# Performance work log

Measured on AMD Instinct MI355X. Metric: run time of the kernel, lower is better.

The kernel has to match this reference:

```python
import jax, jax.numpy as jnp
import numpy as np
from jax import lax

# dims
B, N, D, H, K, NS = 16, 4096, 64, 128, 32, 1024  # clouds, pts/cloud, feat, hidden, max neighbors, fps samples
R = 0.2  # radius


def _fps(pos, n_s):
    """Farthest point sampling on one cloud. pos: [N,3] -> idx [n_s] int32."""
    n = pos.shape[0]

    def step(carry, _):
        dist, last = carry
        d = jnp.sum((pos - pos[last]) ** 2, axis=-1)
        dist = jnp.minimum(dist, d)
        nxt = jnp.argmax(dist).astype(jnp.int32)
        return (dist, nxt), last

    init = (jnp.full((n,), 1e10, pos.dtype), jnp.int32(0))
    _, idx = lax.scan(step, init, None, length=n_s)
    return idx


def setup_inputs() -> dict:
    key = jax.random.key(0)
    ks = jax.random.split(key, 6)
    s1 = 1.0 / np.sqrt(D + 1)
    s2 = 1.0 / np.sqrt(H)
    s3 = 1.0 / np.sqrt(D + H)
    return {
        "x": jax.random.normal(ks[0], (B, N, D), jnp.float32),
        "pos": jax.random.uniform(ks[1], (B, N, 3), jnp.float32),
        "W1": jax.random.normal(ks[2], (D + 1, H), jnp.float32) * s1,
        "b1": jnp.zeros((H,), jnp.float32),
        "W2": jax.random.normal(ks[3], (H, 3), jnp.float32) * s2,
        "b2": jnp.zeros((3,), jnp.float32),
        "W3": jax.random.normal(ks[4], (D + H, H), jnp.float32) * s3,
        "b3": jnp.zeros((H,), jnp.float32),
    }


def reference(x, pos, W1, b1, W2, b2, W3, b3):
    # 1) FPS downsample per cloud -> centers
    idx = jax.vmap(lambda p: _fps(p, NS))(pos)                    # [B,NS]
    pos_s = jax.vmap(lambda p, i: p[i])(pos, idx)                 # [B,NS,3]

    # 2) radius neighbor search: nearest-K within R (<= max_num_neighbors=32)
    d2 = jnp.sum((pos_s[:, :, None, :] - pos[:, None, :, :]) ** 2, axis=-1)  # [B,NS,N]
    masked = jnp.where(d2 <= R * R, d2, jnp.inf)
    neg, nbr = lax.top_k(-masked, K)                              # nearest K
    valid = (-neg) <= R * R                                       # [B,NS,K]

    # 3) gather neighbor features/positions
    x_j = jax.vmap(lambda a, i: a[i])(x, nbr)                     # [B,NS,K,D]
    pos_j = jax.vmap(lambda a, i: a[i])(pos, nbr)                 # [B,NS,K,3]
    diff = pos_j - pos_s[:, :, None, :]                           # pos_j - pos_i
    d2sel = jnp.sum(diff ** 2, axis=-1)
    dist = jnp.where(d2sel > 0, jnp.sqrt(jnp.where(d2sel > 0, d2sel, 1.0)), 0.0)

    # 4) message MLPs
    feat = jnp.concatenate([x_j, dist[..., None]], axis=-1)       # [B,NS,K,D+1]
    emb = jax.nn.relu(feat @ W1 + b1)                             # nn_msg_x
    pw = emb @ W2 + b2                                            # nn_msg_pos
    pmsg = diff * pw

    # 5) masked aggregate: sum for x, mean for pos
    m = valid[..., None].astype(emb.dtype)
    aggr_x = jnp.sum(emb * m, axis=2)                             # [B,NS,H]
    cnt = jnp.maximum(jnp.sum(m, axis=2), 1.0)                    # [B,NS,1]
    aggr_pos = jnp.sum(pmsg * m, axis=2) / cnt                    # [B,NS,3]

    # 6) update
    x_d = jax.vmap(lambda a, i: a[i])(x, idx)                     # [B,NS,D]
    out_x = jax.nn.relu(jnp.concatenate([x_d, aggr_x], axis=-1) @ W3 + b3)
    out_pos = pos_s + aggr_pos
    return out_x, out_pos, idx
```

## Files before the change

### kernel.cpp

```cpp
#include <hip/hip_runtime.h>
#include <math.h>

#define B_ 16
#define N_ 4096
#define D_ 64
#define H_ 128
#define K_ 32
#define NS_ 1024
#define R2_ 0.04f
#define CAP_ 1024

typedef short short8 __attribute__((ext_vector_type(8)));
typedef float f32x4 __attribute__((ext_vector_type(4)));
typedef unsigned short ushort_t;

static __device__ __forceinline__ short f2bf(float f) {
    unsigned u = __float_as_uint(f);
    unsigned r = (u + 0x7FFFu + ((u >> 16) & 1u)) >> 16;
    return (short)r;
}

template<int CTRL, int RM>
static __device__ __forceinline__ unsigned dppmov(unsigned v) {
    return (unsigned)__builtin_amdgcn_update_dpp((int)v, (int)v, CTRL, RM, 0xF, false);
}

#define DPP_FMAX_STEP(CTRL, RM)                                           \
    {                                                                     \
        float n = __uint_as_float(dppmov<CTRL, RM>(__float_as_uint(wm))); \
        wm = fmaxf(wm, n);                                                \
    }

#define DPP_UMIN_STEP(CTRL, RM)                                           \
    {                                                                     \
        unsigned n = dppmov<CTRL, RM>(cand);                              \
        cand = n < cand ? n : cand;                                       \
    }

#define DPP_UMIN_STEP_V(var, CTRL, RM)                                    \
    {                                                                     \
        unsigned n = dppmov<CTRL, RM>(var);                               \
        var = n < var ? n : var;                                          \
    }

__global__ __launch_bounds__(256) void cvt_kernel(
    const float* __restrict__ x, ushort_t* __restrict__ xb)
{
    const size_t i = ((size_t)blockIdx.x * 256 + threadIdx.x) * 8;
    float4 a = *(const float4*)(x + i);
    float4 c = *(const float4*)(x + i + 4);
    short8 o;
    o[0] = f2bf(a.x); o[1] = f2bf(a.y); o[2] = f2bf(a.z); o[3] = f2bf(a.w);
    o[4] = f2bf(c.x); o[5] = f2bf(c.y); o[6] = f2bf(c.z); o[7] = f2bf(c.w);
    *(short8*)(xb + i) = o;
}

__global__ __launch_bounds__(256, 1) void fps_kernel(
    const float* __restrict__ pos, int* __restrict__ idx_i,
    float* __restrict__ idx_f, float* __restrict__ pos_s)
{
    __shared__ float4 lpos4[N_];
    __shared__ float4 sres[NS_];
    __shared__ unsigned long long skey[2][4];
    __shared__ float4 scoord[2][4];
    const int b = blockIdx.x;
    const int t = threadIdx.x;
    const int wv = t >> 6;
    const int lane = t & 63;
    const float* posb = pos + (size_t)b * N_ * 3;
    for (int p = t; p < N_; p += 256)
        lpos4[p] = make_float4(posb[3 * p + 0], posb[3 * p + 1], posb[3 * p + 2], 0.f);
    __syncthreads();

    float px[16], py[16], pz[16], dist[16];
#pragma unroll
    for (int j = 0; j < 16; ++j) {
        float4 v = lpos4[t + 256 * j];
        px[j] = v.x; py[j] = v.y; pz[j] = v.z;
        dist[j] = 1e10f;
    }
    unsigned curidx = 0;
    float4 c0 = lpos4[0];
    float ccx = c0.x, ccy = c0.y, ccz = c0.z;

    for (int ns = 0; ns < NS_; ++ns) {
        if (t == 0)
            sres[ns] = make_float4(ccx, ccy, ccz, __uint_as_float(curidx));
        float bv = -1.f; int bj = 0;
#pragma unroll
        for (int j = 0; j < 16; ++j) {
            float dx = __fsub_rn(px[j], ccx);
            float dy = __fsub_rn(py[j], ccy);
            float dz = __fsub_rn(pz[j], ccz);
            float d2 = __fadd_rn(__fadd_rn(__fmul_rn(dx, dx), __fmul_rn(dy, dy)), __fmul_rn(dz, dz));
            float dn = fminf(dist[j], d2);
            dist[j] = dn;
            bool g = dn > bv;
            bv = g ? dn : bv;
            bj = g ? j : bj;
        }
        float wm = bv;
        DPP_FMAX_STEP(0x111, 0xF)
        DPP_FMAX_STEP(0x112, 0xF)
        DPP_FMAX_STEP(0x114, 0xF)
        DPP_FMAX_STEP(0x118, 0xF)
        DPP_FMAX_STEP(0x142, 0xA)
        DPP_FMAX_STEP(0x143, 0xC)
        const float wavemax = __uint_as_float(
            (unsigned)__builtin_amdgcn_readlane((int)__float_as_uint(wm), 63));
        const unsigned pidx = (unsigned)t + ((unsigned)bj << 8);
        const unsigned long long mask = __ballot(bv == wavemax);
        unsigned widx;
        if (__popcll(mask) == 1) {
            const int wl = __ffsll((long long)mask) - 1;
            widx = (unsigned)__builtin_amdgcn_readlane((int)pidx, wl);
        } else {
            unsigned cand = (bv == wavemax) ? pidx : 0xFFFFFFFFu;
            DPP_UMIN_STEP(0x111, 0xF)
            DPP_UMIN_STEP(0x112, 0xF)
            DPP_UMIN_STEP(0x114, 0xF)
            DPP_UMIN_STEP(0x118, 0xF)
            DPP_UMIN_STEP(0x142, 0xA)
            DPP_UMIN_STEP(0x143, 0xC)
            widx = (unsigned)__builtin_amdgcn_readlane((int)cand, 63);
        }
        float4 wc = lpos4[widx];
        if (lane == 0) {
            skey[ns & 1][wv] = (((unsigned long long)__float_as_uint(wavemax)) << 32)
                             | (unsigned long long)(0xFFFFFFFFu - widx);
            scoord[ns & 1][wv] = wc;
        }
        __syncthreads();
        {
            unsigned sid = (unsigned)(lane & 3);
            unsigned long long skv = skey[ns & 1][sid];
            float4 scv = scoord[ns & 1][sid];
            unsigned kh2 = (unsigned)(skv >> 32), kl2 = (unsigned)skv;
#define SLOT_STEP(CTRL)                                                        \
            {                                                                  \
                unsigned nh = dppmov<CTRL, 0xF>(kh2);                          \
                unsigned nl = dppmov<CTRL, 0xF>(kl2);                          \
                unsigned nsid = dppmov<CTRL, 0xF>(sid);                        \
                unsigned long long nk = (((unsigned long long)nh) << 32) | nl; \
                unsigned long long ok = (((unsigned long long)kh2) << 32) | kl2;\
                if (nk > ok) { kh2 = nh; kl2 = nl; sid = nsid; }               \
            }
            SLOT_STEP(0x101)
            SLOT_STEP(0x102)
#undef SLOT_STEP
            const int slotwin = __builtin_amdgcn_readfirstlane((int)sid);
            curidx = 0xFFFFFFFFu - (unsigned)__builtin_amdgcn_readfirstlane((int)kl2);
            ccx = __uint_as_float((unsigned)__builtin_amdgcn_readlane(
                      (int)__float_as_uint(scv.x), slotwin));
            ccy = __uint_as_float((unsigned)__builtin_amdgcn_readlane(
                      (int)__float_as_uint(scv.y), slotwin));
            ccz = __uint_as_float((unsigned)__builtin_amdgcn_readlane(
                      (int)__float_as_uint(scv.z), slotwin));
        }
    }
    __syncthreads();
    for (int i = t; i < NS_; i += 256) {
        float4 r = sres[i];
        unsigned id = __float_as_uint(r.w);
        idx_i[b * NS_ + i] = (int)id;
        idx_f[b * NS_ + i] = (float)id;
        pos_s[(b * NS_ + i) * 3 + 0] = r.x;
        pos_s[(b * NS_ + i) * 3 + 1] = r.y;
        pos_s[(b * NS_ + i) * 3 + 2] = r.z;
    }
}

__global__ __launch_bounds__(256) void nbr_kernel(
    const float* __restrict__ pos, const float* __restrict__ pos_s,
    int* __restrict__ nbr, float* __restrict__ cntv)
{
    __shared__ unsigned long long ck[4][CAP_];
    const int w = threadIdx.x >> 6;
    const int lane = threadIdx.x & 63;
    const int s = blockIdx.x * 4 + w;
    const int b = s >> 10;
    const float cx = pos_s[s * 3 + 0], cy = pos_s[s * 3 + 1], cz = pos_s[s * 3 + 2];
    const float* posb = pos + (size_t)b * N_ * 3;
    int m = 0;
    for (int base = 0; base < N_; base += 64) {
        int p = base + lane;
        float dx = __fsub_rn(posb[3 * p + 0], cx);
        float dy = __fsub_rn(posb[3 * p + 1], cy);
        float dz = __fsub_rn(posb[3 * p + 2], cz);
        float d2 = __fadd_rn(__fadd_rn(__fmul_rn(dx, dx), __fmul_rn(dy, dy)), __fmul_rn(dz, dz));
        bool in = (d2 <= R2_);
        unsigned long long msk = __ballot(in);
        int before = __popcll(msk & ((1ull << lane) - 1ull));
        int slot = m + before;
        if (in && slot < CAP_)
            ck[w][slot] = ((unsigned long long)__float_as_uint(d2) << 32) | (unsigned)p;
        m += __popcll(msk);
    }
    if (m > CAP_) m = CAP_;
    __asm__ volatile("s_waitcnt lgkmcnt(0)" ::: "memory");
    int kcnt = m < K_ ? m : K_;
    if (m <= 256) {
        unsigned long long kr[4];
#pragma unroll
        for (int r = 0; r < 4; ++r) {
            int q = r * 64 + lane;
            unsigned long long v = ck[w][q & (CAP_ - 1)];
            kr[r] = (q < m) ? v : ~0ull;
        }
        unsigned chosen = 0;
        for (int k = 0; k < kcnt; ++k) {
            unsigned long long localk = ~0ull; int br = -1;
#pragma unroll
            for (int r = 0; r < 4; ++r) {
                bool ok = (!((chosen >> r) & 1u)) && (kr[r] < localk);
                localk = ok ? kr[r] : localk;
                br = ok ? r : br;
            }
            const unsigned mybits = (unsigned)(localk >> 32);
            const unsigned myidx = (unsigned)localk;
            unsigned wb = mybits;
            DPP_UMIN_STEP_V(wb, 0x111, 0xF)
            DPP_UMIN_STEP_V(wb, 0x112, 0xF)
            DPP_UMIN_STEP_V(wb, 0x114, 0xF)
            DPP_UMIN_STEP_V(wb, 0x118, 0xF)
            DPP_UMIN_STEP_V(wb, 0x142, 0xA)
            DPP_UMIN_STEP_V(wb, 0x143, 0xC)
            const unsigned minbits = (unsigned)__builtin_amdgcn_readlane((int)wb, 63);
            const unsigned long long wmask = __ballot(mybits == minbits);
            unsigned widx;
            if (__popcll(wmask) == 1) {
                const int wl = __ffsll((long long)wmask) - 1;
                widx = (unsigned)__builtin_amdgcn_readlane((int)myidx, wl);
            } else {
                unsigned cand = (mybits == minbits) ? myidx : 0xFFFFFFFFu;
                DPP_UMIN_STEP(0x111, 0xF)
                DPP_UMIN_STEP(0x112, 0xF)
                DPP_UMIN_STEP(0x114, 0xF)
                DPP_UMIN_STEP(0x118, 0xF)
                DPP_UMIN_STEP(0x142, 0xA)
                DPP_UMIN_STEP(0x143, 0xC)
                widx = (unsigned)__builtin_amdgcn_readlane((int)cand, 63);
            }
            if (mybits == minbits && myidx == widx) chosen |= 1u << br;
            if (lane == 0) nbr[s * K_ + k] = (int)widx;
        }
    } else {
        unsigned chosen = 0;
        for (int k = 0; k < kcnt; ++k) {
            unsigned long long localk = ~0ull; int bslot = -1;
            for (int r = 0; r * 64 + lane < m; ++r) {
                if (chosen & (1u << r)) continue;
                int q = r * 64 + lane;
                unsigned long long key = ck[w][q];
                if (key < localk) { localk = key; bslot = q; }
            }
            unsigned kh = (unsigned)(localk >> 32), kl = (unsigned)localk;
#define DPP_MIN_STEP2(CTRL, RM)                                           \
            {                                                             \
                unsigned nh = dppmov<CTRL, RM>(kh);                       \
                unsigned nl = dppmov<CTRL, RM>(kl);                       \
                unsigned long long nk = (((unsigned long long)nh) << 32) | nl; \
                unsigned long long ok = (((unsigned long long)kh) << 32) | kl; \
                if (nk < ok) { kh = nh; kl = nl; }                        \
            }
            DPP_MIN_STEP2(0x111, 0xF)
            DPP_MIN_STEP2(0x112, 0xF)
            DPP_MIN_STEP2(0x114, 0xF)
            DPP_MIN_STEP2(0x118, 0xF)
            DPP_MIN_STEP2(0x142, 0xA)
            DPP_MIN_STEP2(0x143, 0xC)
#undef DPP_MIN_STEP2
            unsigned mh = (unsigned)__builtin_amdgcn_readlane((int)kh, 63);
            unsigned ml = (unsigned)__builtin_amdgcn_readlane((int)kl, 63);
            unsigned long long bk = (((unsigned long long)mh) << 32) | ml;
            if (localk == bk && bslot >= 0) chosen |= 1u << (bslot >> 6);
            if (lane == 0) nbr[s * K_ + k] = (int)(bk & 0xFFFFFFFFull);
        }
    }
    if (lane == 0) {
        for (int k = kcnt; k < K_; ++k) nbr[s * K_ + k] = -1;
        cntv[s] = (float)kcnt;
    }
}

__global__ __launch_bounds__(256) void msg_kernel(
    const ushort_t* __restrict__ xb, const float* __restrict__ pos,
    const float* __restrict__ W1, const float* __restrict__ b1,
    const float* __restrict__ W2, const float* __restrict__ b2,
    const float* __restrict__ pos_s, const int* __restrict__ nbr,
    const float* __restrict__ cntv, float* __restrict__ aggr_x,
    float* __restrict__ out_pos)
{
    __shared__ __align__(16) char smem[4 * 5120];
    const int t = threadIdx.x;
    const int wv = t >> 6, lane = t & 63;
    const int quad = lane >> 4, cl = lane & 15;
    char* wb = smem + wv * 5120;

    short8 bfrag[8][2];
    float b1v[8], w1dv[8], w2v0[8], w2v1[8], w2v2[8];
#pragma unroll
    for (int Nt = 0; Nt < 8; ++Nt) {
        const int h = Nt * 16 + cl;
#pragma unroll
        for (int ks = 0; ks < 2; ++ks) {
            short8 f;
#pragma unroll
            for (int jj = 0; jj < 8; ++jj)
                f[jj] = f2bf(W1[(ks * 32 + quad * 8 + jj) * H_ + h]);
            bfrag[Nt][ks] = f;
        }
        b1v[Nt] = b1[h];
        w1dv[Nt] = W1[64 * H_ + h];
        w2v0[Nt] = W2[h * 3 + 0];
        w2v1[Nt] = W2[h * 3 + 1];
        w2v2[Nt] = W2[h * 3 + 2];
    }
    const float b20 = b2[0], b21 = b2[1], b22 = b2[2];

    const int kkg = lane >> 1, half = lane & 1;
    for (int i = 0; i < 4; ++i) {
        const int s = blockIdx.x * 16 + wv * 4 + i;
        const int b = s >> 10;
        const int n = nbr[s * K_ + kkg];
        {
            char* frow = wb + kkg * 144 + half * 64;
            if (n >= 0) {
                const short8* xr = (const short8*)(xb + ((size_t)b * N_ + n) * D_) + half * 4;
#pragma unroll
                for (int q = 0; q < 4; ++q) *(short8*)(frow + q * 16) = xr[q];
            } else {
                short8 z = {0, 0, 0, 0, 0, 0, 0, 0};
#pragma unroll
                for (int q = 0; q < 4; ++q) *(short8*)(frow + q * 16) = z;
            }
            if (half == 0) {
                float dxm = 0.f, dym = 0.f, dzm = 0.f, de = -1.f;
                if (n >= 0) {
                    const float* pj = pos + ((size_t)b * N_ + n) * 3;
                    float dx = pj[0] - pos_s[s * 3 + 0];
                    float dy = pj[1] - pos_s[s * 3 + 1];
                    float dz = pj[2] - pos_s[s * 3 + 2];
                    float d2 = dx * dx + dy * dy + dz * dz;
                    de = d2 > 0.f ? sqrtf(d2) : 0.f;
                    dxm = dx; dym = dy; dzm = dz;
                }
                f32x4 sv = {dxm, dym, dzm, de};
                *(f32x4*)(wb + 4608 + kkg * 16) = sv;
            }
        }
        float agp[8] = {0, 0, 0, 0, 0, 0, 0, 0};
        float gp0[8] = {0, 0, 0, 0, 0, 0, 0, 0};
        float gp1[8] = {0, 0, 0, 0, 0, 0, 0, 0};
        float gp2[8] = {0, 0, 0, 0, 0, 0, 0, 0};
#pragma unroll
        for (int Mt = 0; Mt < 2; ++Mt) {
            short8 a0 = *(short8*)(wb + (Mt * 16 + cl) * 144 + quad * 16);
            short8 a1 = *(short8*)(wb + (Mt * 16 + cl) * 144 + 64 + quad * 16);
            f32x4 acc[8];
#pragma unroll
            for (int Nt = 0; Nt < 8; ++Nt) {
                f32x4 z = {0.f, 0.f, 0.f, 0.f};
                z = __builtin_amdgcn_mfma_f32_16x16x32_bf16(a0, bfrag[Nt][0], z, 0, 0, 0);
                z = __builtin_amdgcn_mfma_f32_16x16x32_bf16(a1, bfrag[Nt][1], z, 0, 0, 0);
                acc[Nt] = z;
            }
            f32x4 sd[4];
#pragma unroll
            for (int r = 0; r < 4; ++r)
                sd[r] = *(f32x4*)(wb + 4608 + (Mt * 16 + quad * 4 + r) * 16);
#pragma unroll
            for (int Nt = 0; Nt < 8; ++Nt) {
#pragma unroll
                for (int r = 0; r < 4; ++r) {
                    float dr = sd[r][3];
                    float wgt = dr >= 0.f ? 1.f : 0.f;
                    float dd = dr >= 0.f ? dr : 0.f;
                    float e = fmaf(dd, w1dv[Nt], acc[Nt][r]) + b1v[Nt];
                    e = e > 0.f ? e : 0.f;
                    agp[Nt] = fmaf(wgt, e, agp[Nt]);
                    gp0[Nt] = fmaf(sd[r][0], e, gp0[Nt]);
                    gp1[Nt] = fmaf(sd[r][1], e, gp1[Nt]);
                    gp2[Nt] = fmaf(sd[r][2], e, gp2[Nt]);
                }
            }
        }
#pragma unroll
        for (int Nt = 0; Nt < 8; ++Nt) {
            float v = agp[Nt]; v += __shfl_xor(v, 16); v += __shfl_xor(v, 32);
            aggr_x[(size_t)s * H_ + Nt * 16 + cl] = v;
            float g0 = gp0[Nt]; g0 += __shfl_xor(g0, 16); g0 += __shfl_xor(g0, 32); gp0[Nt] = g0;
            float g1 = gp1[Nt]; g1 += __shfl_xor(g1, 16); g1 += __shfl_xor(g1, 32); gp1[Nt] = g1;
            float g2 = gp2[Nt]; g2 += __shfl_xor(g2, 16); g2 += __shfl_xor(g2, 32); gp2[Nt] = g2;
        }
        float pr0 = 0.f, pr1 = 0.f, pr2 = 0.f;
#pragma unroll
        for (int Nt = 0; Nt < 8; ++Nt) {
            pr0 = fmaf(w2v0[Nt], gp0[Nt], pr0);
            pr1 = fmaf(w2v1[Nt], gp1[Nt], pr1);
            pr2 = fmaf(w2v2[Nt], gp2[Nt], pr2);
        }
#pragma unroll
        for (int off = 1; off < 16; off <<= 1) {
            pr0 += __shfl_xor(pr0, off);
            pr1 += __shfl_xor(pr1, off);
            pr2 += __shfl_xor(pr2, off);
        }
        f32x4 dsv = *(f32x4*)(wb + 4608 + (lane & 31) * 16);
        float q0 = dsv[0], q1 = dsv[1], q2 = dsv[2];
#pragma unroll
        for (int off = 1; off < 32; off <<= 1) {
            q0 += __shfl_xor(q0, off);
            q1 += __shfl_xor(q1, off);
            q2 += __shfl_xor(q2, off);
        }
        float cnt = cntv[s]; if (cnt < 1.f) cnt = 1.f;
        if (lane < 3) {
            float pr = lane == 0 ? pr0 : (lane == 1 ? pr1 : pr2);
            float qq = lane == 0 ? q0 : (lane == 1 ? q1 : q2);
            float bb = lane == 0 ? b20 : (lane == 1 ? b21 : b22);
            out_pos[s * 3 + lane] = pos_s[s * 3 + lane] + (pr + bb * qq) / cnt;
        }
    }
}

__global__ __launch_bounds__(128) void out_kernel(
    const float* __restrict__ x, const float* __restrict__ W3,
    const float* __restrict__ b3, const int* __restrict__ idx_i,
    const float* __restrict__ aggr_x, float* __restrict__ out_x)
{
    __shared__ float rows[32][208];
    const int t = threadIdx.x;
    const int s0 = blockIdx.x * 32;
    const int sl = t >> 2, part = t & 3;
    const int s = s0 + sl;
    const int b = s >> 10;
    const int id = idx_i[s];
    {
        const float4* xr = (const float4*)(x + ((size_t)b * N_ + id) * D_);
        float4* rr = (float4*)&rows[sl][0];
#pragma unroll
        for (int q = 0; q < 4; ++q) rr[part * 4 + q] = xr[part * 4 + q];
        const float4* ar = (const float4*)(aggr_x + (size_t)s * H_);
        float4* rr2 = (float4*)&rows[sl][64];
#pragma unroll
        for (int q = 0; q < 8; ++q) rr2[part * 8 + q] = ar[part * 8 + q];
    }
    __syncthreads();
    float acc[32];
#pragma unroll
    for (int i = 0; i < 32; ++i) acc[i] = 0.f;
    for (int j4 = 0; j4 < 48; ++j4) {
        float w0 = W3[(j4 * 4 + 0) * H_ + t];
        float w1 = W3[(j4 * 4 + 1) * H_ + t];
        float w2 = W3[(j4 * 4 + 2) * H_ + t];
        float w3 = W3[(j4 * 4 + 3) * H_ + t];
#pragma unroll
        for (int i = 0; i < 32; ++i) {
            const float4 f = *(const float4*)&rows[i][j4 * 4];
            float a = acc[i];
            a = fmaf(f.x, w0, a); a = fmaf(f.y, w1, a);
            a = fmaf(f.z, w2, a); a = fmaf(f.w, w3, a);
            acc[i] = a;
        }
    }
    const float bb = b3[t];
#pragma unroll
    for (int i = 0; i < 32; ++i) {
        float v = acc[i] + bb;
        v = v > 0.f ? v : 0.f;
        out_x[(size_t)(s0 + i) * H_ + t] = v;
    }
}

extern "C" void kernel_launch(void* const* d_in, const int* in_sizes, int n_in,
                              void* d_out, int out_size, void* d_ws, size_t ws_size,
                              hipStream_t stream) {
    const float* x   = (const float*)d_in[0];
    const float* pos = (const float*)d_in[1];
    const float* W1  = (const float*)d_in[2];
    const float* b1  = (const float*)d_in[3];
    const float* W2  = (const float*)d_in[4];
    const float* b2  = (const float*)d_in[5];
    const float* W3  = (const float*)d_in[6];
    const float* b3  = (const float*)d_in[7];

    float* out_x   = (float*)d_out;
    float* out_pos = (float*)d_out + 2097152;
    float* idx_f   = (float*)d_out + 2146304;

    char* ws = (char*)d_ws;
    int*      idx_i  = (int*)ws;
    float*    pos_s  = (float*)(ws + 65536);
    int*      nbr    = (int*)(ws + 262144);
    float*    cntv   = (float*)(ws + 2359296);
    float*    aggr_x = (float*)(ws + 2424832);
    ushort_t* x_bf16 = (ushort_t*)(ws + 10813440);

    cvt_kernel<<<(B_ * N_ * D_) / (256 * 8), 256, 0, stream>>>(x, x_bf16);
    fps_kernel<<<B_, 256, 0, stream>>>(pos, idx_i, idx_f, pos_s);
    nbr_kernel<<<(B_ * NS_) / 4, 256, 0, stream>>>(pos, pos_s, nbr, cntv);
    msg_kernel<<<(B_ * NS_) / 16, 256, 0, stream>>>(x_bf16, pos, W1, b1, W2, b2,
                                                    pos_s, nbr, cntv, aggr_x, out_pos);
    out_kernel<<<(B_ * NS_) / 32, 128, 0, stream>>>(x, W3, b3, idx_i, aggr_x, out_x);
}
```

Baseline: 968.3 us.

## Fuse all stages into a persistent mega-kernel with FPS progress flags

Replaces the five kernel launches with one kernel. A ticket counter assigns the first 16 blocks to FPS, and these publish progress every 64 samples through release atomics. The other 1024 blocks each handle 16 centers and wait on that progress, then run the neighbor search, message MLP and output MLP inside the block. The aim is to overlap the serial FPS with downstream work and to drop the intermediate global buffers (nbr, cntv, aggr_x, bf16 copy of x). In exchange it relies on forward progress of spinning blocks, converts x to bf16 again at every neighbor gather, and runs the output GEMM at lower per-block parallelism.

```diff
diff --git a/kernel.cpp b/kernel.cpp
--- a/kernel.cpp
+++ b/kernel.cpp
@@ -12,7 +12,6 @@
 
 typedef short short8 __attribute__((ext_vector_type(8)));
 typedef float f32x4 __attribute__((ext_vector_type(4)));
-typedef unsigned short ushort_t;
 
 static __device__ __forceinline__ short f2bf(float f) {
     unsigned u = __float_as_uint(f);
@@ -43,196 +42,82 @@
         var = n < var ? n : var;                                          \
     }
 
-__global__ __launch_bounds__(256) void cvt_kernel(
-    const float* __restrict__ x, ushort_t* __restrict__ xb)
+__global__ __launch_bounds__(256, 1) void mega_kernel(
+    const float* __restrict__ pos, const float* __restrict__ x,
+    const float* __restrict__ W1, const float* __restrict__ b1,
+    const float* __restrict__ W2, const float* __restrict__ b2,
+    const float* __restrict__ W3, const float* __restrict__ b3,
+    int* ticket, int* progress, int* idx_i, float* pos_s,
+    float* out_x, float* out_pos, float* idx_f)
 {
-    const size_t i = ((size_t)blockIdx.x * 256 + threadIdx.x) * 8;
-    float4 a = *(const float4*)(x + i);
-    float4 c = *(const float4*)(x + i + 4);
-    short8 o;
-    o[0] = f2bf(a.x); o[1] = f2bf(a.y); o[2] = f2bf(a.z); o[3] = f2bf(a.w);
-    o[4] = f2bf(c.x); o[5] = f2bf(c.y); o[6] = f2bf(c.z); o[7] = f2bf(c.w);
-    *(short8*)(xb + i) = o;
-}
-
-__global__ __launch_bounds__(256, 1) void fps_kernel(
-    const float* __restrict__ pos, int* __restrict__ idx_i,
-    float* __restrict__ idx_f, float* __restrict__ pos_s)
-{
-    __shared__ float4 lpos4[N_];
-    __shared__ float4 sres[NS_];
-    __shared__ unsigned long long skey[2][4];
-    __shared__ float4 scoord[2][4];
-    const int b = blockIdx.x;
+    __shared__ __align__(16) char smem[66048];
+    __shared__ int srole;
     const int t = threadIdx.x;
+    if (t == 0) srole = atomicAdd(ticket, 1);
+    __syncthreads();
+    const int my = srole;
     const int wv = t >> 6;
     const int lane = t & 63;
-    const float* posb = pos + (size_t)b * N_ * 3;
-    for (int p = t; p < N_; p += 256)
-        lpos4[p] = make_float4(posb[3 * p + 0], posb[3 * p + 1], posb[3 * p + 2], 0.f);
-    __syncthreads();
-
-    float px[16], py[16], pz[16], dist[16];
-#pragma unroll
-    for (int j = 0; j < 16; ++j) {
-        float4 v = lpos4[t + 256 * j];
-        px[j] = v.x; py[j] = v.y; pz[j] = v.z;
-        dist[j] = 1e10f;
-    }
-    unsigned curidx = 0;
-    float4 c0 = lpos4[0];
-    float ccx = c0.x, ccy = c0.y, ccz = c0.z;
-
-    for (int ns = 0; ns < NS_; ++ns) {
-        if (t == 0)
-            sres[ns] = make_float4(ccx, ccy, ccz, __uint_as_float(curidx));
-        float bv = -1.f; int bj = 0;
+
+    if (my < B_) {
+        float4* lpos4 = (float4*)smem;
+        unsigned long long (*skey)[4] = (unsigned long long (*)[4])(smem + 65536);
+        float4 (*scoord)[4] = (float4 (*)[4])(smem + 65536 + 64);
+        const int b = my;
+        const float* posb = pos + (size_t)b * N_ * 3;
+        for (int p = t; p < N_; p += 256)
+            lpos4[p] = make_float4(posb[3 * p + 0], posb[3 * p + 1], posb[3 * p + 2], 0.f);
+        __syncthreads();
+
+        float px[16], py[16], pz[16], dist[16];
 #pragma unroll
         for (int j = 0; j < 16; ++j) {
-            float dx = __fsub_rn(px[j], ccx);
-            float dy = __fsub_rn(py[j], ccy);
-            float dz = __fsub_rn(pz[j], ccz);
-            float d2 = __fadd_rn(__fadd_rn(__fmul_rn(dx, dx), __fmul_rn(dy, dy)), __fmul_rn(dz, dz));
-            float dn = fminf(dist[j], d2);
-            dist[j] = dn;
-            bool g = dn > bv;
-            bv = g ? dn : bv;
-            bj = g ? j : bj;
-        }
-        float wm = bv;
-        DPP_FMAX_STEP(0x111, 0xF)
-        DPP_FMAX_STEP(0x112, 0xF)
-        DPP_FMAX_STEP(0x114, 0xF)
-        DPP_FMAX_STEP(0x118, 0xF)
-        DPP_FMAX_STEP(0x142, 0xA)
-        DPP_FMAX_STEP(0x143, 0xC)
-        const float wavemax = __uint_as_float(
-            (unsigned)__builtin_amdgcn_readlane((int)__float_as_uint(wm), 63));
-        const unsigned pidx = (unsigned)t + ((unsigned)bj << 8);
-        const unsigned long long mask = __ballot(bv == wavemax);
-        unsigned widx;
-        if (__popcll(mask) == 1) {
-            const int wl = __ffsll((long long)mask) - 1;
-            widx = (unsigned)__builtin_amdgcn_readlane((int)pidx, wl);
-        } else {
-            unsigned cand = (bv == wavemax) ? pidx : 0xFFFFFFFFu;
-            DPP_UMIN_STEP(0x111, 0xF)
-            DPP_UMIN_STEP(0x112, 0xF)
-            DPP_UMIN_STEP(0x114, 0xF)
-            DPP_UMIN_STEP(0x118, 0xF)
-            DPP_UMIN_STEP(0x142, 0xA)
-            DPP_UMIN_STEP(0x143, 0xC)
-            widx = (unsigned)__builtin_amdgcn_readlane((int)cand, 63);
-        }
-        float4 wc = lpos4[widx];
-        if (lane == 0) {
-            skey[ns & 1][wv] = (((unsigned long long)__float_as_uint(wavemax)) << 32)
-                             | (unsigned long long)(0xFFFFFFFFu - widx);
-            scoord[ns & 1][wv] = wc;
-        }
-        __syncthreads();
-        {
-            unsigned sid = (unsigned)(lane & 3);
-            unsigned long long skv = skey[ns & 1][sid];
-            float4 scv = scoord[ns & 1][sid];
-            unsigned kh2 = (unsigned)(skv >> 32), kl2 = (unsigned)skv;
-#define SLOT_STEP(CTRL)                                                        \
-            {                                                                  \
-                unsigned nh = dppmov<CTRL, 0xF>(kh2);                          \
-                unsigned nl = dppmov<CTRL, 0xF>(kl2);                          \
-                unsigned nsid = dppmov<CTRL, 0xF>(sid);                        \
-                unsigned long long nk = (((unsigned long long)nh) << 32) | nl; \
-                unsigned long long ok = (((unsigned long long)kh2) << 32) | kl2;\
-                if (nk > ok) { kh2 = nh; kl2 = nl; sid = nsid; }               \
-            }
-            SLOT_STEP(0x101)
-            SLOT_STEP(0x102)
-#undef SLOT_STEP
-            const int slotwin = __builtin_amdgcn_readfirstlane((int)sid);
-            curidx = 0xFFFFFFFFu - (unsigned)__builtin_amdgcn_readfirstlane((int)kl2);
-            ccx = __uint_as_float((unsigned)__builtin_amdgcn_readlane(
-                      (int)__float_as_uint(scv.x), slotwin));
-            ccy = __uint_as_float((unsigned)__builtin_amdgcn_readlane(
-                      (int)__float_as_uint(scv.y), slotwin));
-            ccz = __uint_as_float((unsigned)__builtin_amdgcn_readlane(
-                      (int)__float_as_uint(scv.z), slotwin));
-        }
-    }
-    __syncthreads();
-    for (int i = t; i < NS_; i += 256) {
-        float4 r = sres[i];
-        unsigned id = __float_as_uint(r.w);
-        idx_i[b * NS_ + i] = (int)id;
-        idx_f[b * NS_ + i] = (float)id;
-        pos_s[(b * NS_ + i) * 3 + 0] = r.x;
-        pos_s[(b * NS_ + i) * 3 + 1] = r.y;
-        pos_s[(b * NS_ + i) * 3 + 2] = r.z;
-    }
-}
-
-__global__ __launch_bounds__(256) void nbr_kernel(
-    const float* __restrict__ pos, const float* __restrict__ pos_s,
-    int* __restrict__ nbr, float* __restrict__ cntv)
-{
-    __shared__ unsigned long long ck[4][CAP_];
-    const int w = threadIdx.x >> 6;
-    const int lane = threadIdx.x & 63;
-    const int s = blockIdx.x * 4 + w;
-    const int b = s >> 10;
-    const float cx = pos_s[s * 3 + 0], cy = pos_s[s * 3 + 1], cz = pos_s[s * 3 + 2];
-    const float* posb = pos + (size_t)b * N_ * 3;
-    int m = 0;
-    for (int base = 0; base < N_; base += 64) {
-        int p = base + lane;
-        float dx = __fsub_rn(posb[3 * p + 0], cx);
-        float dy = __fsub_rn(posb[3 * p + 1], cy);
-        float dz = __fsub_rn(posb[3 * p + 2], cz);
-        float d2 = __fadd_rn(__fadd_rn(__fmul_rn(dx, dx), __fmul_rn(dy, dy)), __fmul_rn(dz, dz));
-        bool in = (d2 <= R2_);
-        unsigned long long msk = __ballot(in);
-        int before = __popcll(msk & ((1ull << lane) - 1ull));
-        int slot = m + before;
-        if (in && slot < CAP_)
-            ck[w][slot] = ((unsigned long long)__float_as_uint(d2) << 32) | (unsigned)p;
-        m += __popcll(msk);
-    }
-    if (m > CAP_) m = CAP_;
-    __asm__ volatile("s_waitcnt lgkmcnt(0)" ::: "memory");
-    int kcnt = m < K_ ? m : K_;
-    if (m <= 256) {
-        unsigned long long kr[4];
-#pragma unroll
-        for (int r = 0; r < 4; ++r) {
-            int q = r * 64 + lane;
-            unsigned long long v = ck[w][q & (CAP_ - 1)];
-            kr[r] = (q < m) ? v : ~0ull;
-        }
-        unsigned chosen = 0;
-        for (int k = 0; k < kcnt; ++k) {
-            unsigned long long localk = ~0ull; int br = -1;
-#pragma unroll
-            for (int r = 0; r < 4; ++r) {
-                bool ok = (!((chosen >> r) & 1u)) && (kr[r] < localk);
-                localk = ok ? kr[r] : localk;
-                br = ok ? r : br;
-            }
-            const unsigned mybits = (unsigned)(localk >> 32);
-            const unsigned myidx = (unsigned)localk;
-            unsigned wb = mybits;
-            DPP_UMIN_STEP_V(wb, 0x111, 0xF)
-            DPP_UMIN_STEP_V(wb, 0x112, 0xF)
-            DPP_UMIN_STEP_V(wb, 0x114, 0xF)
-            DPP_UMIN_STEP_V(wb, 0x118, 0xF)
-            DPP_UMIN_STEP_V(wb, 0x142, 0xA)
-            DPP_UMIN_STEP_V(wb, 0x143, 0xC)
-            const unsigned minbits = (unsigned)__builtin_amdgcn_readlane((int)wb, 63);
-            const unsigned long long wmask = __ballot(mybits == minbits);
+            float4 v = lpos4[t + 256 * j];
+            px[j] = v.x; py[j] = v.y; pz[j] = v.z;
+            dist[j] = 1e10f;
+        }
+        unsigned curidx = 0;
+        float4 c0 = lpos4[0];
+        float ccx = c0.x, ccy = c0.y, ccz = c0.z;
+
+        for (int ns = 0; ns < NS_; ++ns) {
+            if (t == 0) {
+                idx_i[b * NS_ + ns] = (int)curidx;
+                idx_f[b * NS_ + ns] = (float)curidx;
+                pos_s[(b * NS_ + ns) * 3 + 0] = ccx;
+                pos_s[(b * NS_ + ns) * 3 + 1] = ccy;
+                pos_s[(b * NS_ + ns) * 3 + 2] = ccz;
+            }
+            float bv = -1.f; int bj = 0;
+#pragma unroll
+            for (int j = 0; j < 16; ++j) {
+                float dx = __fsub_rn(px[j], ccx);
+                float dy = __fsub_rn(py[j], ccy);
+                float dz = __fsub_rn(pz[j], ccz);
+                float d2 = __fadd_rn(__fadd_rn(__fmul_rn(dx, dx), __fmul_rn(dy, dy)), __fmul_rn(dz, dz));
+                float dn = fminf(dist[j], d2);
+                dist[j] = dn;
+                bool g = dn > bv;
+                bv = g ? dn : bv;
+                bj = g ? j : bj;
+            }
+            float wm = bv;
+            DPP_FMAX_STEP(0x111, 0xF)
+            DPP_FMAX_STEP(0x112, 0xF)
+            DPP_FMAX_STEP(0x114, 0xF)
+            DPP_FMAX_STEP(0x118, 0xF)
+            DPP_FMAX_STEP(0x142, 0xA)
+            DPP_FMAX_STEP(0x143, 0xC)
+            const float wavemax = __uint_as_float(
+                (unsigned)__builtin_amdgcn_readlane((int)__float_as_uint(wm), 63));
+            const unsigned pidx = (unsigned)t + ((unsigned)bj << 8);
+            const unsigned long long mask = __ballot(bv == wavemax);
             unsigned widx;
-            if (__popcll(wmask) == 1) {
-                const int wl = __ffsll((long long)wmask) - 1;
-                widx = (unsigned)__builtin_amdgcn_readlane((int)myidx, wl);
+            if (__popcll(mask) == 1) {
+                const int wl = __ffsll((long long)mask) - 1;
+                widx = (unsigned)__builtin_amdgcn_readlane((int)pidx, wl);
             } else {
-                unsigned cand = (mybits == minbits) ? myidx : 0xFFFFFFFFu;
+                unsigned cand = (bv == wavemax) ? pidx : 0xFFFFFFFFu;
                 DPP_UMIN_STEP(0x111, 0xF)
                 DPP_UMIN_STEP(0x112, 0xF)
                 DPP_UMIN_STEP(0x114, 0xF)
@@ -241,61 +126,56 @@
                 DPP_UMIN_STEP(0x143, 0xC)
                 widx = (unsigned)__builtin_amdgcn_readlane((int)cand, 63);
             }
-            if (mybits == minbits && myidx == widx) chosen |= 1u << br;
-            if (lane == 0) nbr[s * K_ + k] = (int)widx;
-        }
-    } else {
-        unsigned chosen = 0;
-        for (int k = 0; k < kcnt; ++k) {
-            unsigned long long localk = ~0ull; int bslot = -1;
-            for (int r = 0; r * 64 + lane < m; ++r) {
-                if (chosen & (1u << r)) continue;
-                int q = r * 64 + lane;
-                unsigned long long key = ck[w][q];
-                if (key < localk) { localk = key; bslot = q; }
-            }
-            unsigned kh = (unsigned)(localk >> 32), kl = (unsigned)localk;
-#define DPP_MIN_STEP2(CTRL, RM)                                           \
-            {                                                             \
-                unsigned nh = dppmov<CTRL, RM>(kh);                       \
-                unsigned nl = dppmov<CTRL, RM>(kl);                       \
-                unsigned long long nk = (((unsigned long long)nh) << 32) | nl; \
-                unsigned long long ok = (((unsigned long long)kh) << 32) | kl; \
-                if (nk < ok) { kh = nh; kl = nl; }                        \
-            }
-            DPP_MIN_STEP2(0x111, 0xF)
-            DPP_MIN_STEP2(0x112, 0xF)
-            DPP_MIN_STEP2(0x114, 0xF)
-            DPP_MIN_STEP2(0x118, 0xF)
-            DPP_MIN_STEP2(0x142, 0xA)
-            DPP_MIN_STEP2(0x143, 0xC)
-#undef DPP_MIN_STEP2
-            unsigned mh = (unsigned)__builtin_amdgcn_readlane((int)kh, 63);
-            unsigned ml = (unsigned)__builtin_amdgcn_readlane((int)kl, 63);
-            unsigned long long bk = (((unsigned long long)mh) << 32) | ml;
-            if (localk == bk && bslot >= 0) chosen |= 1u << (bslot >> 6);
-            if (lane == 0) nbr[s * K_ + k] = (int)(bk & 0xFFFFFFFFull);
-        }
-    }
-    if (lane == 0) {
-        for (int k = kcnt; k < K_; ++k) nbr[s * K_ + k] = -1;
-        cntv[s] = (float)kcnt;
-    }
-}
-
-__global__ __launch_bounds__(256) void msg_kernel(
-    const ushort_t* __restrict__ xb, const float* __restrict__ pos,
-    const float* __restrict__ W1, const float* __restrict__ b1,
-    const float* __restrict__ W2, const float* __restrict__ b2,
-    const float* __restrict__ pos_s, const int* __restrict__ nbr,
-    const float* __restrict__ cntv, float* __restrict__ aggr_x,
-    float* __restrict__ out_pos)
-{
-    __shared__ __align__(16) char smem[4 * 5120];
-    const int t = threadIdx.x;
-    const int wv = t >> 6, lane = t & 63;
+            float4 wc = lpos4[widx];
+            if (lane == 0) {
+                skey[ns & 1][wv] = (((unsigned long long)__float_as_uint(wavemax)) << 32)
+                                 | (unsigned long long)(0xFFFFFFFFu - widx);
+                scoord[ns & 1][wv] = wc;
+            }
+            __syncthreads();
+            {
+                unsigned sid = (unsigned)(lane & 3);
+                unsigned long long skv = skey[ns & 1][sid];
+                float4 scv = scoord[ns & 1][sid];
+                unsigned kh2 = (unsigned)(skv >> 32), kl2 = (unsigned)skv;
+#define SLOT_STEP(CTRL)                                                        \
+                {                                                              \
+                    unsigned nh = dppmov<CTRL, 0xF>(kh2);                      \
+                    unsigned nl = dppmov<CTRL, 0xF>(kl2);                      \
+                    unsigned nsid = dppmov<CTRL, 0xF>(sid);                    \
+                    unsigned long long nk = (((unsigned long long)nh) << 32) | nl; \
+                    unsigned long long ok = (((unsigned long long)kh2) << 32) | kl2;\
+                    if (nk > ok) { kh2 = nh; kl2 = nl; sid = nsid; }           \
+                }
+                SLOT_STEP(0x101)
+                SLOT_STEP(0x102)
+#undef SLOT_STEP
+                const int slotwin = __builtin_amdgcn_readfirstlane((int)sid);
+                curidx = 0xFFFFFFFFu - (unsigned)__builtin_amdgcn_readfirstlane((int)kl2);
+                ccx = __uint_as_float((unsigned)__builtin_amdgcn_readlane(
+                          (int)__float_as_uint(scv.x), slotwin));
+                ccy = __uint_as_float((unsigned)__builtin_amdgcn_readlane(
+                          (int)__float_as_uint(scv.y), slotwin));
+                ccz = __uint_as_float((unsigned)__builtin_amdgcn_readlane(
+                          (int)__float_as_uint(scv.z), slotwin));
+            }
+            if (((ns & 63) == 63) && t == 0) {
+                __threadfence();
+                __hip_atomic_store(progress + b, ns + 1,
+                                   __ATOMIC_RELEASE, __HIP_MEMORY_SCOPE_AGENT);
+            }
+        }
+        return;
+    }
+
+    const int wt = my - B_;
+    const int b = wt & 15;
+    const int c = wt >> 4;
+    const int s0 = b * NS_ + c * 16;
     const int quad = lane >> 4, cl = lane & 15;
-    char* wb = smem + wv * 5120;
+    unsigned long long* ckw = (unsigned long long*)smem + (size_t)wv * CAP_;
+    char* wbp = smem + 32768 + wv * 5120;
+    float* rows = (float*)(smem + 53248);
 
     short8 bfrag[8][2];
     float b1v[8], w1dv[8], w2v0[8], w2v1[8], w2v2[8];
@@ -318,17 +198,135 @@
     }
     const float b20 = b2[0], b21 = b2[1], b22 = b2[2];
 
+    if (t == 0) {
+        const int need = c * 16 + 16;
+        while (__hip_atomic_load(progress + b, __ATOMIC_ACQUIRE,
+                                 __HIP_MEMORY_SCOPE_AGENT) < need)
+            __builtin_amdgcn_s_sleep(8);
+    }
+    __syncthreads();
+    __threadfence();
+
+    const volatile float* psv = pos_s;
+    const volatile int*   iiv = idx_i;
+    const float* posb = pos + (size_t)b * N_ * 3;
     const int kkg = lane >> 1, half = lane & 1;
+
     for (int i = 0; i < 4; ++i) {
-        const int s = blockIdx.x * 16 + wv * 4 + i;
-        const int b = s >> 10;
-        const int n = nbr[s * K_ + kkg];
+        const int s = s0 + wv * 4 + i;
+        const int sl = wv * 4 + i;
+        const float cx = psv[s * 3 + 0], cy = psv[s * 3 + 1], cz = psv[s * 3 + 2];
+        int m = 0;
+        for (int base = 0; base < N_; base += 64) {
+            int p = base + lane;
+            float dx = __fsub_rn(posb[3 * p + 0], cx);
+            float dy = __fsub_rn(posb[3 * p + 1], cy);
+            float dz = __fsub_rn(posb[3 * p + 2], cz);
+            float d2 = __fadd_rn(__fadd_rn(__fmul_rn(dx, dx), __fmul_rn(dy, dy)), __fmul_rn(dz, dz));
+            bool in = (d2 <= R2_);
+            unsigned long long msk = __ballot(in);
+            int before = __popcll(msk & ((1ull << lane) - 1ull));
+            int slot = m + before;
+            if (in && slot < CAP_)
+                ckw[slot] = ((unsigned long long)__float_as_uint(d2) << 32) | (unsigned)p;
+            m += __popcll(msk);
+        }
+        if (m > CAP_) m = CAP_;
+        __asm__ volatile("s_waitcnt lgkmcnt(0)" ::: "memory");
+        const int kcnt = m < K_ ? m : K_;
+        int nidx = -1;
+        if (m <= 256) {
+            unsigned long long kr[4];
+#pragma unroll
+            for (int r = 0; r < 4; ++r) {
+                int q = r * 64 + lane;
+                unsigned long long v = ckw[q & (CAP_ - 1)];
+                kr[r] = (q < m) ? v : ~0ull;
+            }
+            unsigned chosen = 0;
+            for (int k = 0; k < kcnt; ++k) {
+                unsigned long long localk = ~0ull; int br = -1;
+#pragma unroll
+                for (int r = 0; r < 4; ++r) {
+                    bool ok = (!((chosen >> r) & 1u)) && (kr[r] < localk);
+                    localk = ok ? kr[r] : localk;
+                    br = ok ? r : br;
+                }
+                const unsigned mybits = (unsigned)(localk >> 32);
+                const unsigned myidx = (unsigned)localk;
+                unsigned wb2 = mybits;
+                DPP_UMIN_STEP_V(wb2, 0x111, 0xF)
+                DPP_UMIN_STEP_V(wb2, 0x112, 0xF)
+                DPP_UMIN_STEP_V(wb2, 0x114, 0xF)
+                DPP_UMIN_STEP_V(wb2, 0x118, 0xF)
+                DPP_UMIN_STEP_V(wb2, 0x142, 0xA)
+                DPP_UMIN_STEP_V(wb2, 0x143, 0xC)
+                const unsigned minbits = (unsigned)__builtin_amdgcn_readlane((int)wb2, 63);
+                const unsigned long long wmask = __ballot(mybits == minbits);
+                unsigned widx;
+                if (__popcll(wmask) == 1) {
+                    const int wl = __ffsll((long long)wmask) - 1;
+                    widx = (unsigned)__builtin_amdgcn_readlane((int)myidx, wl);
+                } else {
+                    unsigned cand = (mybits == minbits) ? myidx : 0xFFFFFFFFu;
+                    DPP_UMIN_STEP(0x111, 0xF)
+                    DPP_UMIN_STEP(0x112, 0xF)
+                    DPP_UMIN_STEP(0x114, 0xF)
+                    DPP_UMIN_STEP(0x118, 0xF)
+                    DPP_UMIN_STEP(0x142, 0xA)
+                    DPP_UMIN_STEP(0x143, 0xC)
+                    widx = (unsigned)__builtin_amdgcn_readlane((int)cand, 63);
+                }
+                if (mybits == minbits && myidx == widx) chosen |= 1u << br;
+                if (kkg == k) nidx = (int)widx;
+            }
+        } else {
+            unsigned chosen = 0;
+            for (int k = 0; k < kcnt; ++k) {
+                unsigned long long localk = ~0ull; int bslot = -1;
+                for (int r = 0; r * 64 + lane < m; ++r) {
+                    if (chosen & (1u << r)) continue;
+                    int q = r * 64 + lane;
+                    unsigned long long key = ckw[q];
+                    if (key < localk) { localk = key; bslot = q; }
+                }
+                unsigned kh = (unsigned)(localk >> 32), kl = (unsigned)localk;
+#define DPP_MIN_STEP2(CTRL, RM)                                               \
+                {                                                             \
+                    unsigned nh = dppmov<CTRL, RM>(kh);                       \
+                    unsigned nl = dppmov<CTRL, RM>(kl);                       \
+                    unsigned long long nk = (((unsigned long long)nh) << 32) | nl; \
+                    unsigned long long ok = (((unsigned long long)kh) << 32) | kl; \
+                    if (nk < ok) { kh = nh; kl = nl; }                        \
+                }
+                DPP_MIN_STEP2(0x111, 0xF)
+                DPP_MIN_STEP2(0x112, 0xF)
+                DPP_MIN_STEP2(0x114, 0xF)
+                DPP_MIN_STEP2(0x118, 0xF)
+                DPP_MIN_STEP2(0x142, 0xA)
+                DPP_MIN_STEP2(0x143, 0xC)
+#undef DPP_MIN_STEP2
+                unsigned mh = (unsigned)__builtin_amdgcn_readlane((int)kh, 63);
+                unsigned ml = (unsigned)__builtin_amdgcn_readlane((int)kl, 63);
+                unsigned long long bk = (((unsigned long long)mh) << 32) | ml;
+                if (localk == bk && bslot >= 0) chosen |= 1u << (bslot >> 6);
+                if (kkg == k) nidx = (int)(bk & 0xFFFFFFFFull);
+            }
+        }
+        const float cnt = (kcnt < 1) ? 1.f : (float)kcnt;
         {
-            char* frow = wb + kkg * 144 + half * 64;
+            char* frow = wbp + kkg * 144 + half * 64;
+            const int n = nidx;
             if (n >= 0) {
-                const short8* xr = (const short8*)(xb + ((size_t)b * N_ + n) * D_) + half * 4;
-#pragma unroll
-                for (int q = 0; q < 4; ++q) *(short8*)(frow + q * 16) = xr[q];
+                const float4* xr = (const float4*)(x + ((size_t)b * N_ + n) * D_) + half * 8;
+#pragma unroll
+                for (int q = 0; q < 4; ++q) {
+                    float4 a = xr[q * 2], cc = xr[q * 2 + 1];
+                    short8 o;
+                    o[0] = f2bf(a.x); o[1] = f2bf(a.y); o[2] = f2bf(a.z); o[3] = f2bf(a.w);
+                    o[4] = f2bf(cc.x); o[5] = f2bf(cc.y); o[6] = f2bf(cc.z); o[7] = f2bf(cc.w);
+                    *(short8*)(frow + q * 16) = o;
+                }
             } else {
                 short8 z = {0, 0, 0, 0, 0, 0, 0, 0};
 #pragma unroll
@@ -338,15 +336,15 @@
                 float dxm = 0.f, dym = 0.f, dzm = 0.f, de = -1.f;
                 if (n >= 0) {
                     const float* pj = pos + ((size_t)b * N_ + n) * 3;
-                    float dx = pj[0] - pos_s[s * 3 + 0];
-                    float dy = pj[1] - pos_s[s * 3 + 1];
-                    float dz = pj[2] - pos_s[s * 3 + 2];
+                    float dx = pj[0] - cx;
+                    float dy = pj[1] - cy;
+                    float dz = pj[2] - cz;
                     float d2 = dx * dx + dy * dy + dz * dz;
                     de = d2 > 0.f ? sqrtf(d2) : 0.f;
                     dxm = dx; dym = dy; dzm = dz;
                 }
                 f32x4 sv = {dxm, dym, dzm, de};
-                *(f32x4*)(wb + 4608 + kkg * 16) = sv;
+                *(f32x4*)(wbp + 4608 + kkg * 16) = sv;
             }
         }
         float agp[8] = {0, 0, 0, 0, 0, 0, 0, 0};
@@ -355,8 +353,8 @@
         float gp2[8] = {0, 0, 0, 0, 0, 0, 0, 0};
 #pragma unroll
         for (int Mt = 0; Mt < 2; ++Mt) {
-            short8 a0 = *(short8*)(wb + (Mt * 16 + cl) * 144 + quad * 16);
-            short8 a1 = *(short8*)(wb + (Mt * 16 + cl) * 144 + 64 + quad * 16);
+            short8 a0 = *(short8*)(wbp + (Mt * 16 + cl) * 144 + quad * 16);
+            short8 a1 = *(short8*)(wbp + (Mt * 16 + cl) * 144 + 64 + quad * 16);
             f32x4 acc[8];
 #pragma unroll
             for (int Nt = 0; Nt < 8; ++Nt) {
@@ -368,7 +366,7 @@
             f32x4 sd[4];
 #pragma unroll
             for (int r = 0; r < 4; ++r)
-                sd[r] = *(f32x4*)(wb + 4608 + (Mt * 16 + quad * 4 + r) * 16);
+                sd[r] = *(f32x4*)(wbp + 4608 + (Mt * 16 + quad * 4 + r) * 16);
 #pragma unroll
             for (int Nt = 0; Nt < 8; ++Nt) {
 #pragma unroll
@@ -388,7 +386,7 @@
 #pragma unroll
         for (int Nt = 0; Nt < 8; ++Nt) {
             float v = agp[Nt]; v += __shfl_xor(v, 16); v += __shfl_xor(v, 32);
-            aggr_x[(size_t)s * H_ + Nt * 16 + cl] = v;
+            if (quad == 0) rows[sl * 200 + 64 + Nt * 16 + cl] = v;
             float g0 = gp0[Nt]; g0 += __shfl_xor(g0, 16); g0 += __shfl_xor(g0, 32); gp0[Nt] = g0;
             float g1 = gp1[Nt]; g1 += __shfl_xor(g1, 16); g1 += __shfl_xor(g1, 32); gp1[Nt] = g1;
             float g2 = gp2[Nt]; g2 += __shfl_xor(g2, 16); g2 += __shfl_xor(g2, 32); gp2[Nt] = g2;
@@ -406,7 +404,7 @@
             pr1 += __shfl_xor(pr1, off);
             pr2 += __shfl_xor(pr2, off);
         }
-        f32x4 dsv = *(f32x4*)(wb + 4608 + (lane & 31) * 16);
+        f32x4 dsv = *(f32x4*)(wbp + 4608 + (lane & 31) * 16);
         float q0 = dsv[0], q1 = dsv[1], q2 = dsv[2];
 #pragma unroll
         for (int off = 1; off < 32; off <<= 1) {
@@ -414,62 +412,48 @@
             q1 += __shfl_xor(q1, off);
             q2 += __shfl_xor(q2, off);
         }
-        float cnt = cntv[s]; if (cnt < 1.f) cnt = 1.f;
         if (lane < 3) {
             float pr = lane == 0 ? pr0 : (lane == 1 ? pr1 : pr2);
             float qq = lane == 0 ? q0 : (lane == 1 ? q1 : q2);
             float bb = lane == 0 ? b20 : (lane == 1 ? b21 : b22);
-            out_pos[s * 3 + lane] = pos_s[s * 3 + lane] + (pr + bb * qq) / cnt;
-        }
-    }
-}
-
-__global__ __launch_bounds__(128) void out_kernel(
-    const float* __restrict__ x, const float* __restrict__ W3,
-    const float* __restrict__ b3, const int* __restrict__ idx_i,
-    const float* __restrict__ aggr_x, float* __restrict__ out_x)
-{
-    __shared__ float rows[32][208];
-    const int t = threadIdx.x;
-    const int s0 = blockIdx.x * 32;
-    const int sl = t >> 2, part = t & 3;
-    const int s = s0 + sl;
-    const int b = s >> 10;
-    const int id = idx_i[s];
+            out_pos[s * 3 + lane] = psv[s * 3 + lane] + (pr + bb * qq) / cnt;
+        }
+    }
+    __syncthreads();
     {
+        const int sl = t >> 4, part = t & 15;
+        const int id = iiv[s0 + sl];
         const float4* xr = (const float4*)(x + ((size_t)b * N_ + id) * D_);
-        float4* rr = (float4*)&rows[sl][0];
-#pragma unroll
-        for (int q = 0; q < 4; ++q) rr[part * 4 + q] = xr[part * 4 + q];
-        const float4* ar = (const float4*)(aggr_x + (size_t)s * H_);
-        float4* rr2 = (float4*)&rows[sl][64];
-#pragma unroll
-        for (int q = 0; q < 8; ++q) rr2[part * 8 + q] = ar[part * 8 + q];
+        *(float4*)&rows[sl * 200 + part * 4] = xr[part];
     }
     __syncthreads();
-    float acc[32];
-#pragma unroll
-    for (int i = 0; i < 32; ++i) acc[i] = 0.f;
-    for (int j4 = 0; j4 < 48; ++j4) {
-        float w0 = W3[(j4 * 4 + 0) * H_ + t];
-        float w1 = W3[(j4 * 4 + 1) * H_ + t];
-        float w2 = W3[(j4 * 4 + 2) * H_ + t];
-        float w3 = W3[(j4 * 4 + 3) * H_ + t];
-#pragma unroll
-        for (int i = 0; i < 32; ++i) {
-            const float4 f = *(const float4*)&rows[i][j4 * 4];
-            float a = acc[i];
-            a = fmaf(f.x, w0, a); a = fmaf(f.y, w1, a);
-            a = fmaf(f.z, w2, a); a = fmaf(f.w, w3, a);
-            acc[i] = a;
-        }
-    }
-    const float bb = b3[t];
-#pragma unroll
-    for (int i = 0; i < 32; ++i) {
-        float v = acc[i] + bb;
-        v = v > 0.f ? v : 0.f;
-        out_x[(size_t)(s0 + i) * H_ + t] = v;
+    {
+        const int hhalf = t >> 7, h = t & 127;
+        const int r0 = hhalf * 8;
+        float acc[8];
+#pragma unroll
+        for (int r = 0; r < 8; ++r) acc[r] = 0.f;
+        for (int j4 = 0; j4 < 48; ++j4) {
+            float w0 = W3[(j4 * 4 + 0) * H_ + h];
+            float w1 = W3[(j4 * 4 + 1) * H_ + h];
+            float w2 = W3[(j4 * 4 + 2) * H_ + h];
+            float w3 = W3[(j4 * 4 + 3) * H_ + h];
+#pragma unroll
+            for (int r = 0; r < 8; ++r) {
+                const float4 f = *(const float4*)&rows[(r0 + r) * 200 + j4 * 4];
+                float a = acc[r];
+                a = fmaf(f.x, w0, a); a = fmaf(f.y, w1, a);
+                a = fmaf(f.z, w2, a); a = fmaf(f.w, w3, a);
+                acc[r] = a;
+            }
+        }
+        const float bb = b3[h];
+#pragma unroll
+        for (int r = 0; r < 8; ++r) {
+            float v = acc[r] + bb;
+            v = v > 0.f ? v : 0.f;
+            out_x[(size_t)(s0 + r0 + r) * H_ + h] = v;
+        }
     }
 }
 
@@ -490,17 +474,13 @@
     float* idx_f   = (float*)d_out + 2146304;
 
     char* ws = (char*)d_ws;
-    int*      idx_i  = (int*)ws;
-    float*    pos_s  = (float*)(ws + 65536);
-    int*      nbr    = (int*)(ws + 262144);
-    float*    cntv   = (float*)(ws + 2359296);
-    float*    aggr_x = (float*)(ws + 2424832);
-    ushort_t* x_bf16 = (ushort_t*)(ws + 10813440);
-
-    cvt_kernel<<<(B_ * N_ * D_) / (256 * 8), 256, 0, stream>>>(x, x_bf16);
-    fps_kernel<<<B_, 256, 0, stream>>>(pos, idx_i, idx_f, pos_s);
-    nbr_kernel<<<(B_ * NS_) / 4, 256, 0, stream>>>(pos, pos_s, nbr, cntv);
-    msg_kernel<<<(B_ * NS_) / 16, 256, 0, stream>>>(x_bf16, pos, W1, b1, W2, b2,
-                                                    pos_s, nbr, cntv, aggr_x, out_pos);
-    out_kernel<<<(B_ * NS_) / 32, 128, 0, stream>>>(x, W3, b3, idx_i, aggr_x, out_x);
+    int*   ticket   = (int*)ws;
+    int*   progress = (int*)(ws + 64);
+    float* pos_s    = (float*)(ws + 1024);
+    int*   idx_i    = (int*)(ws + 1024 + 196608);
+
+    hipMemsetAsync(ws, 0, 256, stream);
+    mega_kernel<<<B_ + 1024, 256, 0, stream>>>(pos, x, W1, b1, W2, b2, W3, b3,
+                                               ticket, progress, idx_i, pos_s,
+                                               out_x, out_pos, idx_f);
 }
```

Measured after the change: 1.050 ms. 8.4% more time.
